# Performance work log

Hardware: AMD Instinct MI355X
Metric: run time of the kernel (lower is better)

## Reference

```python
import jax, jax.numpy as jnp
import numpy as np
from jax import lax

B, DIM, H, W = 32, 256, 56, 56
HID = 4 * DIM
EPS = 1e-6


def setup_inputs() -> dict:
    key = jax.random.key(0)
    ks = jax.random.split(key, 8)
    x = jax.random.normal(ks[0], (B, DIM, H, W), dtype=jnp.float32)
    # depthwise conv: OIHW with feature_group_count=DIM -> [DIM, 1, 7, 7]
    conv_w = jax.random.normal(ks[1], (DIM, 1, 7, 7), dtype=jnp.float32) * 0.05
    conv_b = jax.random.normal(ks[2], (DIM,), dtype=jnp.float32) * 0.01
    ln_g = jnp.ones((DIM,), dtype=jnp.float32)
    ln_b = jnp.zeros((DIM,), dtype=jnp.float32)
    w1 = jax.random.normal(ks[3], (DIM, HID), dtype=jnp.float32) * (1.0 / np.sqrt(DIM))
    b1 = jax.random.normal(ks[4], (HID,), dtype=jnp.float32) * 0.01
    w2 = jax.random.normal(ks[5], (HID, DIM), dtype=jnp.float32) * (1.0 / np.sqrt(HID))
    b2 = jax.random.normal(ks[6], (DIM,), dtype=jnp.float32) * 0.01
    return {"x": x, "conv_w": conv_w, "conv_b": conv_b, "ln_g": ln_g,
            "ln_b": ln_b, "w1": w1, "b1": b1, "w2": w2, "b2": b2}


def reference(x, conv_w, conv_b, ln_g, ln_b, w1, b1, w2, b2):
    dim = x.shape[1]
    # 7x7 depthwise conv, stride 1, padding 3 (NCHW)
    y = lax.conv_general_dilated(
        x, conv_w, window_strides=(1, 1), padding=((3, 3), (3, 3)),
        dimension_numbers=("NCHW", "OIHW", "NCHW"), feature_group_count=dim)
    y = y + conv_b[None, :, None, None]
    # permute to NHWC
    y = jnp.transpose(y, (0, 2, 3, 1))  # [B, H, W, C]
    # LayerNorm over channel (last) dim, eps=1e-6, affine
    mu = jnp.mean(y, axis=-1, keepdims=True)
    var = jnp.mean(jnp.square(y - mu), axis=-1, keepdims=True)
    y = (y - mu) * lax.rsqrt(var + EPS) * ln_g + ln_b
    # MLP: Linear -> exact GELU -> Linear
    h = jax.nn.gelu(jnp.einsum("bhwc,cf->bhwf", y, w1) + b1, approximate=False)
    y = jnp.einsum("bhwf,fc->bhwc", h, w2) + b2
    # permute back to NCHW; stochastic depth is identity at eval time
    return jnp.transpose(y, (0, 3, 1, 2))
```

## Files before the change

kernel.cpp:

```cpp
#include <hip/hip_runtime.h>
#include <math.h>

#define CDIM 256
#define HW 3136
#define HID 1024

typedef __attribute__((ext_vector_type(4))) float f32x4;
typedef __attribute__((ext_vector_type(8))) short bf16x8;
typedef __attribute__((ext_vector_type(4))) short bf16x4;

__device__ __forceinline__ unsigned short f2bf(float f){
  unsigned int u = __float_as_uint(f);
  u += 0x7FFFu + ((u >> 16) & 1u);
  return (unsigned short)(u >> 16);
}

__device__ __forceinline__ void load_lds16(const void* g, void* l){
  __builtin_amdgcn_global_load_lds(
      (const __attribute__((address_space(1))) unsigned int*)g,
      (__attribute__((address_space(3))) unsigned int*)l, 16, 0, 0);
}

__global__ __launch_bounds__(256) void prep_kernel(
    const float* __restrict__ w1, const float* __restrict__ w2,
    unsigned short* __restrict__ w1t, unsigned short* __restrict__ w2t){
  __shared__ unsigned short sh[64][70];
  int blk = blockIdx.x;
  const float* src; unsigned short* dst; int M, N, tm, tn;
  if (blk < 64){ src = w1; dst = w1t; M = 256;  N = 1024; tm = blk >> 4; tn = blk & 15; }
  else { blk -= 64; src = w2; dst = w2t; M = 1024; N = 256;  tm = blk >> 2; tn = blk & 3; }
  const int t = threadIdx.x;

  {
    const int r = t >> 4, c4 = t & 15;
    #pragma unroll
    for (int rr = 0; rr < 4; ++rr){
      int row = rr * 16 + r;
      f32x4 v = *(const f32x4*)(src + (long)(tm * 64 + row) * N + tn * 64 + c4 * 4);
      #pragma unroll
      for (int k = 0; k < 4; ++k) sh[row][c4 * 4 + k] = f2bf(v[k]);
    }
  }
  __syncthreads();

  {
    const int n = t >> 2, seg = t & 3;
    bf16x8 o0, o1;
    #pragma unroll
    for (int j = 0; j < 8; ++j){
      o0[j] = (short)sh[seg * 16 + j][n];
      o1[j] = (short)sh[seg * 16 + 8 + j][n];
    }
    unsigned short* dp = dst + (long)(tn * 64 + n) * M + tm * 64 + seg * 16;
    *(bf16x8*)(dp) = o0;
    *(bf16x8*)(dp + 8) = o1;
  }
}

__global__ __launch_bounds__(256) void convln_kernel(
    const float* __restrict__ x, const float* __restrict__ cw,
    const float* __restrict__ cb, const float* __restrict__ lng,
    const float* __restrict__ lnb, unsigned short* __restrict__ y){
  __shared__ float tile[256 * 61];
  __shared__ float part_s[4][64];
  __shared__ float part_q[4][64];
  __shared__ float lg_s[256];
  __shared__ float lb_s[256];

  const int t = threadIdx.x;
  const int blk0 = blockIdx.x;
  const int blk = (blk0 & 7) * 224 + (blk0 >> 3);
  const int b = blk / 56;
  const int h = blk - b * 56;
  const int c = t;

  lg_s[t] = lng[t];
  lb_s[t] = lnb[t];

  float acc[56];
  {
    float bias = cb[c];
    #pragma unroll
    for (int w = 0; w < 56; ++w) acc[w] = bias;
  }

  const float* xim = x + (long)(b * 256 + c) * HW;
  const float* cwc = cw + c * 49;
  for (int i = 0; i < 7; ++i){
    int hh = h - 3 + i;
    if (hh >= 0 && hh < 56){
      float seg[62];
      seg[0] = seg[1] = seg[2] = 0.f;
      seg[59] = seg[60] = seg[61] = 0.f;
      const float* xrow = xim + hh * 56;
      #pragma unroll
      for (int w4 = 0; w4 < 14; ++w4){
        f32x4 v = *(const f32x4*)(xrow + w4 * 4);
        seg[3 + w4 * 4 + 0] = v[0];
        seg[3 + w4 * 4 + 1] = v[1];
        seg[3 + w4 * 4 + 2] = v[2];
        seg[3 + w4 * 4 + 3] = v[3];
      }
      float wt7[7];
      #pragma unroll
      for (int j = 0; j < 7; ++j) wt7[j] = cwc[i * 7 + j];
      #pragma unroll
      for (int j = 0; j < 7; ++j){
        float wj = wt7[j];
        #pragma unroll
        for (int w = 0; w < 56; ++w)
          acc[w] = fmaf(seg[w + j], wj, acc[w]);
      }
    }
  }

  #pragma unroll
  for (int p = 0; p < 56; ++p) tile[c * 61 + p] = acc[p];
  __syncthreads();

  {
    int p = t & 63; if (p > 55) p = 55;
    const int q = t >> 6;
    float s = 0.f, qq = 0.f;
    #pragma unroll 8
    for (int j = 0; j < 64; ++j){
      float v = tile[(q * 64 + j) * 61 + p];
      s += v; qq = fmaf(v, v, qq);
    }
    part_s[q][p] = s;
    part_q[q][p] = qq;
  }
  __syncthreads();

  if (t < 224){
    const int p = t >> 2, c0 = (t & 3) * 64;
    float S = part_s[0][p] + part_s[1][p] + part_s[2][p] + part_s[3][p];
    float Q = part_q[0][p] + part_q[1][p] + part_q[2][p] + part_q[3][p];
    float mu = S * (1.0f / 256.0f);
    float var = Q * (1.0f / 256.0f) - mu * mu;
    float rs = rsqrtf(var + 1e-6f);
    long pos = (long)blk * 56 + p;
    int m7 = (int)(pos & 7);
    unsigned short* yp = y + pos * 256 + c0;
    #pragma unroll
    for (int j = 0; j < 8; ++j){
      bf16x8 o;
      #pragma unroll
      for (int k = 0; k < 8; ++k){
        int cc = c0 + j * 8 + k;
        float v = tile[cc * 61 + p];
        o[k] = (short)f2bf((v - mu) * rs * lg_s[cc] + lb_s[cc]);
      }
      *(bf16x8*)(yp + (j ^ m7) * 8) = o;
    }
  }
}

#define LDS_H0 32768
#define MLP_LDS (32768 + 18432)

__global__ __launch_bounds__(256, 3) void mlp_kernel(
    const unsigned short* __restrict__ y, const unsigned short* __restrict__ w1t,
    const unsigned short* __restrict__ w2t, const float* __restrict__ b1,
    const float* __restrict__ b2, float* __restrict__ out){
  __shared__ __align__(16) unsigned char smem[MLP_LDS];
  const int t = threadIdx.x;
  const int wv = t >> 6, lane = t & 63;
  const int lr = lane & 15, lq = lane >> 4;
  const int r7 = lr & 7;
  const int blk = blockIdx.x;

  {
    const unsigned char* ybase = (const unsigned char*)(y + (long)blk * 64 * 256);
    #pragma unroll
    for (int r = 0; r < 8; ++r){
      int g = wv * 8 + r;
      load_lds16(ybase + g * 1024 + lane * 16, smem + g * 1024);
    }
  }

  bf16x8 wf[8];
  {
    const unsigned short* w1p = w1t + ((wv * 16 + lr) << 8);
    #pragma unroll
    for (int ks = 0; ks < 8; ++ks)
      wf[ks] = *(const bf16x8*)(w1p + ks * 32 + lq * 8);
  }

  f32x4 acc2[4][4];
  #pragma unroll
  for (int a = 0; a < 4; ++a)
    #pragma unroll
    for (int bb = 0; bb < 4; ++bb) acc2[a][bb] = (f32x4){0.f, 0.f, 0.f, 0.f};

  __syncthreads();

  for (int ch = 0; ch < 16; ++ch){
    unsigned char* Hbuf = smem + LDS_H0 + (ch & 1) * 9216;

    f32x4 acc1[4];
    #pragma unroll
    for (int mt = 0; mt < 4; ++mt) acc1[mt] = (f32x4){0.f, 0.f, 0.f, 0.f};
    #pragma unroll
    for (int ks = 0; ks < 8; ++ks){
      bf16x8 yf[4];
      #pragma unroll
      for (int mt = 0; mt < 4; ++mt){
        int jl = ks * 4 + lq;
        int ofs = (mt * 16 + lr) * 512 + (((jl & 24) | ((jl ^ r7) & 7)) << 4);
        yf[mt] = *(const bf16x8*)(smem + ofs);
      }
      #pragma unroll
      for (int mt = 0; mt < 4; ++mt)
        acc1[mt] = __builtin_amdgcn_mfma_f32_16x16x32_bf16(wf[ks], yf[mt], acc1[mt], 0, 0, 0);
    }

    bf16x8 w2f[2][4];
    #pragma unroll
    for (int ks2 = 0; ks2 < 2; ++ks2)
      #pragma unroll
      for (int ct = 0; ct < 4; ++ct)
        w2f[ks2][ct] = *(const bf16x8*)(w2t + (long)(wv * 64 + ct * 16 + lr) * 1024
                                        + ch * 64 + ks2 * 32 + lq * 8);

    {
      f32x4 bv = *(const f32x4*)(b1 + ch * 64 + wv * 16 + lq * 4);
      #pragma unroll
      for (int mt = 0; mt < 4; ++mt){
        bf16x4 hv;
        #pragma unroll
        for (int r = 0; r < 4; ++r){
          float pv = acc1[mt][r] + bv[r];
          float p2 = pv * pv;
          float u  = pv * fmaf(0.044715f, p2, 1.0f);
          float e  = __builtin_amdgcn_exp2f(-2.3022083f * u);
          float gl = pv * __builtin_amdgcn_rcpf(1.0f + e);
          hv[r] = (short)f2bf(gl);
        }
        *(bf16x4*)(Hbuf + (mt * 16 + lr) * 144 + wv * 32 + lq * 8) = hv;
      }
    }

    {
      int chn = (ch + 1) & 15;
      const unsigned short* w1p = w1t + (((chn * 64) + wv * 16 + lr) << 8);
      #pragma unroll
      for (int ks = 0; ks < 8; ++ks)
        wf[ks] = *(const bf16x8*)(w1p + ks * 32 + lq * 8);
    }

    asm volatile("s_waitcnt lgkmcnt(0)" ::: "memory");
    __builtin_amdgcn_sched_barrier(0);
    __builtin_amdgcn_s_barrier();

    #pragma unroll
    for (int ks2 = 0; ks2 < 2; ++ks2){
      bf16x8 hf[4];
      #pragma unroll
      for (int mt = 0; mt < 4; ++mt)
        hf[mt] = *(const bf16x8*)(Hbuf + (mt * 16 + lr) * 144 + ks2 * 64 + lq * 16);
      #pragma unroll
      for (int ct = 0; ct < 4; ++ct)
        #pragma unroll
        for (int mt = 0; mt < 4; ++mt)
          acc2[ct][mt] = __builtin_amdgcn_mfma_f32_16x16x32_bf16(w2f[ks2][ct], hf[mt], acc2[ct][mt], 0, 0, 0);
    }
  }

  #pragma unroll
  for (int ct = 0; ct < 4; ++ct){
    int cb = wv * 64 + ct * 16 + lq * 4;
    f32x4 b2v = *(const f32x4*)(b2 + cb);
    #pragma unroll
    for (int mt = 0; mt < 4; ++mt){
      int m = mt * 16 + lr;
      unsigned pos = (unsigned)(blk * 64 + m);
      unsigned bimg = pos / 3136u;
      unsigned hw = pos - bimg * 3136u;
      float* op = out + ((long)bimg * 256 + cb) * 3136 + hw;
      #pragma unroll
      for (int r = 0; r < 4; ++r)
        op[r * 3136] = acc2[ct][mt][r] + b2v[r];
    }
  }
}

extern "C" void kernel_launch(void* const* d_in, const int* in_sizes, int n_in,
                              void* d_out, int out_size, void* d_ws, size_t ws_size,
                              hipStream_t stream){
  const float* x  = (const float*)d_in[0];
  const float* cw = (const float*)d_in[1];
  const float* cb = (const float*)d_in[2];
  const float* lg = (const float*)d_in[3];
  const float* lb = (const float*)d_in[4];
  const float* w1 = (const float*)d_in[5];
  const float* b1 = (const float*)d_in[6];
  const float* w2 = (const float*)d_in[7];
  const float* b2 = (const float*)d_in[8];
  float* out = (float*)d_out;

  unsigned short* y   = (unsigned short*)d_ws;
  unsigned short* w1t = (unsigned short*)((char*)d_ws + 51380224);
  unsigned short* w2t = (unsigned short*)((char*)d_ws + 51904512);

  hipLaunchKernelGGL(prep_kernel,   dim3(128),  dim3(256), 0, stream, w1, w2, w1t, w2t);
  hipLaunchKernelGGL(convln_kernel, dim3(1792), dim3(256), 0, stream, x, cw, cb, lg, lb, y);
  hipLaunchKernelGGL(mlp_kernel,    dim3(1568), dim3(256), 0, stream, y, w1t, w2t, b1, b2, out);
}
```

Before: 491.4 us.

## Chunk conv+LayerNorm epilogue through small LDS tile and split row loads

The conv+LN kernel now stages its 56 output positions through LDS in four chunks of 14 instead of one 256x61 tile. This cuts shared memory per block from about 62KB to about 15KB, so more blocks can be resident on a CU. Each input row is also loaded as two overlapping half-segments, which shrinks the live register array. The per-chunk LN output is written by 16 threads per position, each storing two 16B pieces, which makes stores more contiguous. In exchange the epilogue needs extra __syncthreads and repeated small reductions, and the 56-float accumulator still keeps register pressure high.

Measured after the change: 505.2 us. 1.03x slower.

```diff
diff --git a/kernel.cpp b/kernel.cpp
--- a/kernel.cpp
+++ b/kernel.cpp
@@ -61,9 +61,9 @@
     const float* __restrict__ x, const float* __restrict__ cw,
     const float* __restrict__ cb, const float* __restrict__ lng,
     const float* __restrict__ lnb, unsigned short* __restrict__ y){
-  __shared__ float tile[256 * 61];
-  __shared__ float part_s[4][64];
-  __shared__ float part_q[4][64];
+  __shared__ float tile[256 * 15];
+  __shared__ float part_s[16][16];
+  __shared__ float part_q[16][16];
   __shared__ float lg_s[256];
   __shared__ float lb_s[256];
 
@@ -89,69 +89,98 @@
   for (int i = 0; i < 7; ++i){
     int hh = h - 3 + i;
     if (hh >= 0 && hh < 56){
-      float seg[62];
-      seg[0] = seg[1] = seg[2] = 0.f;
-      seg[59] = seg[60] = seg[61] = 0.f;
       const float* xrow = xim + hh * 56;
-      #pragma unroll
-      for (int w4 = 0; w4 < 14; ++w4){
-        f32x4 v = *(const f32x4*)(xrow + w4 * 4);
-        seg[3 + w4 * 4 + 0] = v[0];
-        seg[3 + w4 * 4 + 1] = v[1];
-        seg[3 + w4 * 4 + 2] = v[2];
-        seg[3 + w4 * 4 + 3] = v[3];
-      }
       float wt7[7];
       #pragma unroll
       for (int j = 0; j < 7; ++j) wt7[j] = cwc[i * 7 + j];
-      #pragma unroll
-      for (int j = 0; j < 7; ++j){
-        float wj = wt7[j];
-        #pragma unroll
-        for (int w = 0; w < 56; ++w)
-          acc[w] = fmaf(seg[w + j], wj, acc[w]);
-      }
-    }
-  }
-
-  #pragma unroll
-  for (int p = 0; p < 56; ++p) tile[c * 61 + p] = acc[p];
-  __syncthreads();
-
-  {
-    int p = t & 63; if (p > 55) p = 55;
-    const int q = t >> 6;
-    float s = 0.f, qq = 0.f;
-    #pragma unroll 8
-    for (int j = 0; j < 64; ++j){
-      float v = tile[(q * 64 + j) * 61 + p];
-      s += v; qq = fmaf(v, v, qq);
-    }
-    part_s[q][p] = s;
-    part_q[q][p] = qq;
-  }
-  __syncthreads();
-
-  if (t < 224){
-    const int p = t >> 2, c0 = (t & 3) * 64;
-    float S = part_s[0][p] + part_s[1][p] + part_s[2][p] + part_s[3][p];
-    float Q = part_q[0][p] + part_q[1][p] + part_q[2][p] + part_q[3][p];
-    float mu = S * (1.0f / 256.0f);
-    float var = Q * (1.0f / 256.0f) - mu * mu;
-    float rs = rsqrtf(var + 1e-6f);
-    long pos = (long)blk * 56 + p;
-    int m7 = (int)(pos & 7);
-    unsigned short* yp = y + pos * 256 + c0;
-    #pragma unroll
-    for (int j = 0; j < 8; ++j){
-      bf16x8 o;
+
+      {
+        float sa[35];
+        sa[0] = sa[1] = sa[2] = 0.f;
+        #pragma unroll
+        for (int v4 = 0; v4 < 8; ++v4){
+          f32x4 v = *(const f32x4*)(xrow + v4 * 4);
+          sa[3 + v4 * 4 + 0] = v[0];
+          sa[3 + v4 * 4 + 1] = v[1];
+          sa[3 + v4 * 4 + 2] = v[2];
+          sa[3 + v4 * 4 + 3] = v[3];
+        }
+        #pragma unroll
+        for (int j = 0; j < 7; ++j){
+          float wj = wt7[j];
+          #pragma unroll
+          for (int w = 0; w < 28; ++w)
+            acc[w] = fmaf(sa[w + j], wj, acc[w]);
+        }
+      }
+      {
+        float sb[35];
+        sb[32] = sb[33] = sb[34] = 0.f;
+        #pragma unroll
+        for (int v4 = 0; v4 < 8; ++v4){
+          f32x4 v = *(const f32x4*)(xrow + 24 + v4 * 4);
+          sb[v4 * 4 + 0] = v[0];
+          sb[v4 * 4 + 1] = v[1];
+          sb[v4 * 4 + 2] = v[2];
+          sb[v4 * 4 + 3] = v[3];
+        }
+        #pragma unroll
+        for (int j = 0; j < 7; ++j){
+          float wj = wt7[j];
+          #pragma unroll
+          for (int w = 28; w < 56; ++w)
+            acc[w] = fmaf(sb[w + j - 27], wj, acc[w]);
+        }
+      }
+    }
+  }
+
+  for (int ck = 0; ck < 4; ++ck){
+    const int p0 = ck * 14;
+    __syncthreads();
+    #pragma unroll
+    for (int dp = 0; dp < 14; ++dp) tile[c * 15 + dp] = acc[p0 + dp];
+    __syncthreads();
+
+    {
+      const int dp = t & 15, cg = t >> 4;
+      if (dp < 14){
+        float s = 0.f, q = 0.f;
+        #pragma unroll
+        for (int j = 0; j < 16; ++j){
+          float v = tile[(cg * 16 + j) * 15 + dp];
+          s += v; q = fmaf(v, v, q);
+        }
+        part_s[cg][dp] = s;
+        part_q[cg][dp] = q;
+      }
+    }
+    __syncthreads();
+
+    if (t < 224){
+      const int pp = t >> 4;
+      const int cs = t & 15;
+      float S = 0.f, Q = 0.f;
+      #pragma unroll
+      for (int g = 0; g < 16; ++g){ S += part_s[g][pp]; Q += part_q[g][pp]; }
+      float mu = S * (1.0f / 256.0f);
+      float var = Q * (1.0f / 256.0f) - mu * mu;
+      float rs = rsqrtf(var + 1e-6f);
+      long pos = (long)blk * 56 + p0 + pp;
+      int m7 = (int)(pos & 7);
+      int c0 = cs * 16;
+      bf16x8 o0, o1;
       #pragma unroll
       for (int k = 0; k < 8; ++k){
-        int cc = c0 + j * 8 + k;
-        float v = tile[cc * 61 + p];
-        o[k] = (short)f2bf((v - mu) * rs * lg_s[cc] + lb_s[cc]);
-      }
-      *(bf16x8*)(yp + (j ^ m7) * 8) = o;
+        float v0 = tile[(c0 + k) * 15 + pp];
+        float v1 = tile[(c0 + 8 + k) * 15 + pp];
+        o0[k] = (short)f2bf((v0 - mu) * rs * lg_s[c0 + k] + lb_s[c0 + k]);
+        o1[k] = (short)f2bf((v1 - mu) * rs * lg_s[c0 + 8 + k] + lb_s[c0 + 8 + k]);
+      }
+      unsigned short* yp = y + pos * 256;
+      int j0 = cs * 2;
+      *(bf16x8*)(yp + ((j0 ^ m7) << 3)) = o0;
+      *(bf16x8*)(yp + (((j0 + 1) ^ m7) << 3)) = o1;
     }
   }
 }
```
